# Kernel tuning notes

Measured on AMD Instinct MI355X. Metric: run time of the kernel, lower is better.

## Reference

```python
import jax, jax.numpy as jnp
import numpy as np

DIM = 1024
HEADS = 16
DIM_HEAD = 64
DIM_INNER = HEADS * DIM_HEAD  # 1024


def setup_inputs() -> dict:
    key = jax.random.key(0)
    k1, k2, k3 = jax.random.split(key, 3)
    x = jax.random.normal(k1, (2, 2048, DIM), dtype=jnp.float32)
    gamma = jnp.zeros((DIM,), dtype=jnp.float32)  # init as in module
    # store weights as [in, out] so y = x @ W (equivalent to torch Linear with W.T)
    w_qkv = jax.random.normal(k2, (DIM, DIM_INNER * 3), dtype=jnp.float32) * (DIM ** -0.5)
    w_out = jax.random.normal(k3, (DIM_INNER, DIM), dtype=jnp.float32) * (DIM_INNER ** -0.5)
    return {"x": x, "gamma": gamma, "w_qkv": w_qkv, "w_out": w_out}


def rms_norm(x, gamma):
    # F.normalize(x, dim=-1) * sqrt(dim) * (gamma + 1)
    eps = 1e-12
    norm = jnp.maximum(jnp.linalg.norm(x, axis=-1, keepdims=True), eps)
    return x / norm * (x.shape[-1] ** 0.5) * (gamma + 1.0)


def reference(x, gamma, w_qkv, w_out):
    b, n, _ = x.shape
    scale = DIM_HEAD ** -0.5
    xn = rms_norm(x, gamma)
    qkv = xn @ w_qkv  # [b, n, 3*h*d]
    qkv = qkv.reshape(b, n, 3, HEADS, DIM_HEAD)
    qkv = jnp.transpose(qkv, (2, 0, 3, 1, 4))  # [3, b, h, n, d]
    q, k, v = qkv[0], qkv[1], qkv[2]
    q = q * scale
    sim = jnp.einsum('bhid,bhjd->bhij', q, k)
    attn = jax.nn.softmax(sim, axis=-1)
    out = jnp.einsum('bhij,bhjd->bhid', attn, v)  # [b, h, n, d]
    out = jnp.transpose(out, (0, 2, 1, 3)).reshape(b, n, DIM_INNER)
    return out @ w_out
```

## Files before the change

kernel.cpp:

```cpp
#include <hip/hip_runtime.h>
#include <hip/hip_bf16.h>
#include <string.h>

typedef unsigned short ushort_t;
typedef __attribute__((ext_vector_type(8))) short short8;
typedef __attribute__((ext_vector_type(4))) short short4v;
typedef __attribute__((ext_vector_type(4))) float floatx4;
typedef __attribute__((ext_vector_type(4))) int int4v;
typedef __attribute__((ext_vector_type(4))) unsigned short us4;

#define MFMA(a, b, c) __builtin_amdgcn_mfma_f32_16x16x32_bf16(a, b, c, 0, 0, 0)
#define MFMA16(a, b, c) __builtin_amdgcn_mfma_f32_16x16x16bf16_1k(a, b, c, 0, 0, 0)

__device__ __forceinline__ float b2f(ushort_t u) {
    union { float f; unsigned i; } c; c.i = ((unsigned)u) << 16; return c.f;
}
__device__ __forceinline__ ushort_t f2b(float f) {
    union { float f; unsigned i; } c; c.f = f;
    unsigned r = c.i + 0x7FFFu + ((c.i >> 16) & 1u);
    return (ushort_t)(r >> 16);
}
__device__ __forceinline__ unsigned pk_bf16(float a, float b) {
    float2 f; f.x = a; f.y = b;
    __hip_bfloat162 h = __float22bfloat162_rn(f);
    unsigned u;
    memcpy(&u, &h, 4);
    return u;
}
__device__ __forceinline__ void gl_lds16(const ushort_t* g, ushort_t* l) {
    __builtin_amdgcn_global_load_lds(
        (const __attribute__((address_space(1))) void*)g,
        (__attribute__((address_space(3))) void*)l, 16, 0, 0);
}

__global__ __launch_bounds__(256) void rmsnorm_k(const float* __restrict__ x,
                                                 const float* __restrict__ gamma,
                                                 ushort_t* __restrict__ xn) {
    int row = blockIdx.x;
    const float* xr = x + (size_t)row * 1024;
    ushort_t* orow = xn + (size_t)row * 1024;
    int t = threadIdx.x;

    floatx4 u = *(const floatx4*)&xr[t * 4];
    float ss = u[0] * u[0] + u[1] * u[1] + u[2] * u[2] + u[3] * u[3];
    #pragma unroll
    for (int off = 32; off; off >>= 1) ss += __shfl_xor(ss, off);
    __shared__ float red[4];
    if ((t & 63) == 0) red[t >> 6] = ss;
    __syncthreads();
    float tot = red[0] + red[1] + red[2] + red[3];
    float inv = rsqrtf(fmaxf(tot, 1e-24f)) * 32.0f;

    floatx4 g = *(const floatx4*)&gamma[t * 4];
    us4 o;
    o.x = f2b(u[0] * inv * (1.0f + g[0]));
    o.y = f2b(u[1] * inv * (1.0f + g[1]));
    o.z = f2b(u[2] * inv * (1.0f + g[2]));
    o.w = f2b(u[3] * inv * (1.0f + g[3]));
    *(us4*)&orow[t * 4] = o;
}

__global__ __launch_bounds__(256) void transpose_cvt2_k(const float* __restrict__ wq,
                                                        ushort_t* __restrict__ oq,
                                                        const float* __restrict__ wo,
                                                        ushort_t* __restrict__ oo) {
    __shared__ ushort_t Ts[64 * 72];
    int bid = blockIdx.x;
    const float* in; ushort_t* out; int K, N, n0, k0;
    if (bid < 768) { in = wq; out = oq; K = 1024; N = 3072;
                     n0 = (bid % 48) * 64; k0 = (bid / 48) * 64; }
    else           { int b2 = bid - 768; in = wo; out = oo; K = 1024; N = 1024;
                     n0 = (b2 & 15) * 64; k0 = (b2 >> 4) * 64; }
    int t = threadIdx.x;
    #pragma unroll
    for (int i = 0; i < 4; i++) {
        int idx = t + i * 256;
        int r = idx >> 4, g = idx & 15;
        floatx4 v = *(const floatx4*)&in[(size_t)(k0 + r) * N + n0 + g * 4];
        us4 o; o.x = f2b(v[0]); o.y = f2b(v[1]); o.z = f2b(v[2]); o.w = f2b(v[3]);
        *(us4*)&Ts[r * 72 + g * 4] = o;
    }
    __syncthreads();
    #pragma unroll
    for (int i = 0; i < 2; i++) {
        int idx = t + i * 256;
        int r = idx >> 3, g = idx & 7;
        ushort_t tmp[8];
        #pragma unroll
        for (int j = 0; j < 8; j++) tmp[j] = Ts[(g * 8 + j) * 72 + r];
        *(int4v*)&out[(size_t)(n0 + r) * K + k0 + g * 8] = *(const int4v*)tmp;
    }
}

template <bool F32OUT>
__global__ __launch_bounds__(256) void gemm_tn(const ushort_t* __restrict__ A,
                                               const ushort_t* __restrict__ Bt,
                                               void* __restrict__ Cv,
                                               int M, int N, int K) {
    __shared__ ushort_t As[128 * 64];
    __shared__ ushort_t Bs[128 * 64];
    int t = threadIdx.x;
    int m0 = blockIdx.y * 128, n0 = blockIdx.x * 128;
    int lane = t & 63, wave = t >> 6, quad = lane >> 4, l16 = lane & 15;
    int wm = (wave & 1) * 64, wn = (wave >> 1) * 64;
    floatx4 acc[4][4] = {};

    int srow = lane >> 3;
    int schunk = (lane & 7) ^ srow;
    const ushort_t* Ag = A + (size_t)(m0 + wave * 8 + srow) * K + schunk * 8;
    const ushort_t* Bg = Bt + (size_t)(n0 + wave * 8 + srow) * K + schunk * 8;
    int lbase = (wave * 8) * 64;

    int xq = l16 & 7;

    for (int k1 = 0; k1 < K; k1 += 64) {
        #pragma unroll
        for (int i = 0; i < 4; i++) {
            gl_lds16(Ag + (size_t)(i * 32) * K + k1, &As[lbase + i * 32 * 64]);
            gl_lds16(Bg + (size_t)(i * 32) * K + k1, &Bs[lbase + i * 32 * 64]);
        }
        __syncthreads();
        #pragma unroll
        for (int ks = 0; ks < 2; ks++) {
            int ca = ((ks * 4 + quad) ^ xq) * 8;
            short8 af[4], bf[4];
            #pragma unroll
            for (int i = 0; i < 4; i++) {
                af[i] = *(const short8*)&As[(wm + i * 16 + l16) * 64 + ca];
                bf[i] = *(const short8*)&Bs[(wn + i * 16 + l16) * 64 + ca];
            }
            #pragma unroll
            for (int mt = 0; mt < 4; mt++)
                #pragma unroll
                for (int nt = 0; nt < 4; nt++)
                    acc[mt][nt] = MFMA(af[mt], bf[nt], acc[mt][nt]);
        }
        __syncthreads();
    }
    #pragma unroll
    for (int mt = 0; mt < 4; mt++)
        #pragma unroll
        for (int r = 0; r < 4; r++) {
            int row = m0 + wm + mt * 16 + quad * 4 + r;
            #pragma unroll
            for (int nt = 0; nt < 4; nt++) {
                int col = n0 + wn + nt * 16 + l16;
                if constexpr (F32OUT)
                    ((float*)Cv)[(size_t)row * N + col] = acc[mt][nt][r];
                else
                    ((ushort_t*)Cv)[(size_t)row * N + col] = f2b(acc[mt][nt][r]);
            }
        }
}

#define LDA 72
__global__ __launch_bounds__(256, 2) void attn_k(const ushort_t* __restrict__ qk,
                                                 const ushort_t* __restrict__ vT,
                                                 ushort_t* __restrict__ o) {
    __shared__ ushort_t Ks[64 * LDA];
    __shared__ ushort_t Vt[64 * LDA];
    int t = threadIdx.x;
    int lane = t & 63, wave = t >> 6, quad = lane >> 4, l16 = lane & 15;
    int bid = blockIdx.x;
    int bh = bid & 31, qb = bid >> 5;
    int b = bh >> 4, h = bh & 15;
    int q0 = qb * 128 + wave * 32;
    const size_t RS = 2048;
    const ushort_t* Qb = qk + (size_t)b * 2048 * RS + h * 64;
    const ushort_t* Kb = Qb + 1024;
    const ushort_t* Vb = vT + (size_t)(h * 64) * 4096 + b * 2048;
    const float SC = 0.18033688011112042f;

    int srow = t >> 2, sseg = t & 3;
    const ushort_t* Kg = Kb + (size_t)srow * RS + sseg * 8;
    const ushort_t* Vg = Vb + (size_t)srow * 4096 + sseg * 8;

    short8 qf[2][2];
    #pragma unroll
    for (int qt = 0; qt < 2; qt++)
        #pragma unroll
        for (int ks = 0; ks < 2; ks++) {
            union { short8 s; ushort_t u[8]; } a;
            a.s = *(const short8*)&Qb[(size_t)(q0 + qt * 16 + l16) * RS + ks * 32 + quad * 8];
            #pragma unroll
            for (int j = 0; j < 8; j++) a.u[j] = f2b(b2f(a.u[j]) * SC);
            qf[qt][ks] = a.s;
        }

    short4v ones4;
    #pragma unroll
    for (int j = 0; j < 4; j++) ones4[j] = (short)0x3F80;

    floatx4 oacc[2][4] = {};
    floatx4 sum_acc[2] = {};

    int4v kr0 = *(const int4v*)Kg;
    int4v kr1 = *(const int4v*)(Kg + 32);
    int4v vr0 = *(const int4v*)Vg;
    int4v vr1 = *(const int4v*)(Vg + 32);

    for (int kt = 0; kt < 2048; kt += 64) {
        __syncthreads();
        *(int4v*)&Ks[srow * LDA + sseg * 8] = kr0;
        *(int4v*)&Ks[srow * LDA + 32 + sseg * 8] = kr1;
        *(int4v*)&Vt[srow * LDA + sseg * 8] = vr0;
        *(int4v*)&Vt[srow * LDA + 32 + sseg * 8] = vr1;
        __syncthreads();

        if (kt + 64 < 2048) {
            const ushort_t* Kg2 = Kg + (size_t)(kt + 64) * RS;
            const ushort_t* Vg2 = Vg + (kt + 64);
            kr0 = *(const int4v*)Kg2;
            kr1 = *(const int4v*)(Kg2 + 32);
            vr0 = *(const int4v*)Vg2;
            vr1 = *(const int4v*)(Vg2 + 32);
        }

        floatx4 s[2][4];
        #pragma unroll
        for (int mt = 0; mt < 4; mt++) {
            short8 kf0 = *(const short8*)&Ks[(mt * 16 + l16) * LDA + quad * 8];
            short8 kf1 = *(const short8*)&Ks[(mt * 16 + l16) * LDA + 32 + quad * 8];
            #pragma unroll
            for (int qt = 0; qt < 2; qt++) {
                floatx4 z = {};
                z = MFMA(kf0, qf[qt][0], z);
                s[qt][mt] = MFMA(kf1, qf[qt][1], z);
            }
        }

        short4v pa[2][4];
        #pragma unroll
        for (int qt = 0; qt < 2; qt++)
            #pragma unroll
            for (int mt = 0; mt < 4; mt++) {
                union { short4v v; unsigned u[2]; } pk;
                pk.u[0] = pk_bf16(exp2f(s[qt][mt][0]), exp2f(s[qt][mt][1]));
                pk.u[1] = pk_bf16(exp2f(s[qt][mt][2]), exp2f(s[qt][mt][3]));
                pa[qt][mt] = pk.v;
            }

        #pragma unroll
        for (int mt = 0; mt < 4; mt++) {
            short4v vb[4];
            #pragma unroll
            for (int dt = 0; dt < 4; dt++)
                vb[dt] = *(const short4v*)&Vt[(dt * 16 + l16) * LDA + mt * 16 + quad * 4];
            #pragma unroll
            for (int qt = 0; qt < 2; qt++) {
                sum_acc[qt] = MFMA16(pa[qt][mt], ones4, sum_acc[qt]);
                #pragma unroll
                for (int dt = 0; dt < 4; dt++)
                    oacc[qt][dt] = MFMA16(pa[qt][mt], vb[dt], oacc[qt][dt]);
            }
        }
    }

    ushort_t* ob = o + (size_t)b * 2048 * 1024 + h * 64;
    #pragma unroll
    for (int qt = 0; qt < 2; qt++)
        #pragma unroll
        for (int r = 0; r < 4; r++) {
            float inv = 1.0f / sum_acc[qt][r];
            int row = q0 + qt * 16 + quad * 4 + r;
            #pragma unroll
            for (int dt = 0; dt < 4; dt++)
                ob[(size_t)row * 1024 + dt * 16 + l16] = f2b(oacc[qt][dt][r] * inv);
        }
}

extern "C" void kernel_launch(void* const* d_in, const int* in_sizes, int n_in,
                              void* d_out, int out_size, void* d_ws, size_t ws_size,
                              hipStream_t stream) {
    const float* x     = (const float*)d_in[0];
    const float* gamma = (const float*)d_in[1];
    const float* w_qkv = (const float*)d_in[2];
    const float* w_out = (const float*)d_in[3];
    float* out = (float*)d_out;

    ushort_t* ws   = (ushort_t*)d_ws;
    ushort_t* xn   = ws;
    ushort_t* qkb  = xn + (size_t)4096 * 1024;
    ushort_t* vTb  = qkb + (size_t)4096 * 2048;
    ushort_t* wtq  = vTb + (size_t)1024 * 4096;
    ushort_t* wto  = wtq + (size_t)3072 * 1024;
    ushort_t* attn = xn;

    rmsnorm_k<<<4096, 256, 0, stream>>>(x, gamma, xn);
    transpose_cvt2_k<<<1024, 256, 0, stream>>>(w_qkv, wtq, w_out, wto);
    gemm_tn<false><<<dim3(16, 32), 256, 0, stream>>>(xn, wtq, qkb, 4096, 2048, 1024);
    gemm_tn<false><<<dim3(32, 8), 256, 0, stream>>>(wtq + (size_t)2048 * 1024, xn, vTb,
                                                    1024, 4096, 1024);
    attn_k<<<512, 256, 0, stream>>>(qkb, vTb, attn);
    gemm_tn<true><<<dim3(8, 32), 256, 0, stream>>>(attn, wto, out, 4096, 1024, 1024);
}
```

Measured before the change: 218.8 us.

## Fuse QKV GEMM, transpose V separately, split attention keys across two wave groups

```diff
diff --git a/kernel.cpp b/kernel.cpp
--- a/kernel.cpp
+++ b/kernel.cpp
@@ -92,6 +92,32 @@
     }
 }
 
+__global__ __launch_bounds__(256) void transpose_v_k(const ushort_t* __restrict__ qkv,
+                                                     ushort_t* __restrict__ vT) {
+    __shared__ ushort_t Ts[64 * 72];
+    int t = threadIdx.x;
+    int t0 = blockIdx.x * 64;
+    int c0 = blockIdx.y * 64;
+    const ushort_t* in = qkv + 2048 + c0;
+    #pragma unroll
+    for (int i = 0; i < 2; i++) {
+        int idx = t + i * 256;
+        int r = idx >> 3, g = idx & 7;
+        *(int4v*)&Ts[r * 72 + g * 8] =
+            *(const int4v*)&in[(size_t)(t0 + r) * 3072 + g * 8];
+    }
+    __syncthreads();
+    #pragma unroll
+    for (int i = 0; i < 2; i++) {
+        int idx = t + i * 256;
+        int r = idx >> 3, g = idx & 7;
+        ushort_t tmp[8];
+        #pragma unroll
+        for (int j = 0; j < 8; j++) tmp[j] = Ts[(g * 8 + j) * 72 + r];
+        *(int4v*)&vT[(size_t)(c0 + r) * 4096 + t0 + g * 8] = *(const int4v*)tmp;
+    }
+}
+
 template <bool F32OUT>
 __global__ __launch_bounds__(256) void gemm_tn(const ushort_t* __restrict__ A,
                                                const ushort_t* __restrict__ Bt,
@@ -110,7 +136,6 @@
     const ushort_t* Ag = A + (size_t)(m0 + wave * 8 + srow) * K + schunk * 8;
     const ushort_t* Bg = Bt + (size_t)(n0 + wave * 8 + srow) * K + schunk * 8;
     int lbase = (wave * 8) * 64;
-
     int xq = l16 & 7;
 
     for (int k1 = 0; k1 < K; k1 += 64) {
@@ -154,26 +179,31 @@
 }
 
 #define LDA 72
-__global__ __launch_bounds__(256, 2) void attn_k(const ushort_t* __restrict__ qk,
+__global__ __launch_bounds__(512, 4) void attn_k(const ushort_t* __restrict__ qkv,
                                                  const ushort_t* __restrict__ vT,
                                                  ushort_t* __restrict__ o) {
-    __shared__ ushort_t Ks[64 * LDA];
-    __shared__ ushort_t Vt[64 * LDA];
+    __shared__ ushort_t S[4][64 * LDA];
     int t = threadIdx.x;
     int lane = t & 63, wave = t >> 6, quad = lane >> 4, l16 = lane & 15;
+    int half = wave >> 2, w4 = wave & 3;
     int bid = blockIdx.x;
     int bh = bid & 31, qb = bid >> 5;
     int b = bh >> 4, h = bh & 15;
-    int q0 = qb * 128 + wave * 32;
-    const size_t RS = 2048;
-    const ushort_t* Qb = qk + (size_t)b * 2048 * RS + h * 64;
+    int q0 = qb * 128 + w4 * 32;
+    const size_t RS = 3072;
+    const ushort_t* Qb = qkv + (size_t)b * 2048 * RS + h * 64;
     const ushort_t* Kb = Qb + 1024;
     const ushort_t* Vb = vT + (size_t)(h * 64) * 4096 + b * 2048;
     const float SC = 0.18033688011112042f;
 
-    int srow = t >> 2, sseg = t & 3;
-    const ushort_t* Kg = Kb + (size_t)srow * RS + sseg * 8;
-    const ushort_t* Vg = Vb + (size_t)srow * 4096 + sseg * 8;
+    ushort_t* Ks = S[half * 2];
+    ushort_t* Vt = S[half * 2 + 1];
+
+    int ht = t & 255;
+    int srow = ht >> 2, sseg = ht & 3;
+    int kbase = half * 1024;
+    const ushort_t* Kg = Kb + (size_t)(kbase + srow) * RS + sseg * 8;
+    const ushort_t* Vg = Vb + (size_t)srow * 4096 + kbase + sseg * 8;
 
     short8 qf[2][2];
     #pragma unroll
@@ -199,7 +229,7 @@
     int4v vr0 = *(const int4v*)Vg;
     int4v vr1 = *(const int4v*)(Vg + 32);
 
-    for (int kt = 0; kt < 2048; kt += 64) {
+    for (int kt = 0; kt < 1024; kt += 64) {
         __syncthreads();
         *(int4v*)&Ks[srow * LDA + sseg * 8] = kr0;
         *(int4v*)&Ks[srow * LDA + 32 + sseg * 8] = kr1;
@@ -207,7 +237,7 @@
         *(int4v*)&Vt[srow * LDA + 32 + sseg * 8] = vr1;
         __syncthreads();
 
-        if (kt + 64 < 2048) {
+        if (kt + 64 < 1024) {
             const ushort_t* Kg2 = Kg + (size_t)(kt + 64) * RS;
             const ushort_t* Vg2 = Vg + (kt + 64);
             kr0 = *(const int4v*)Kg2;
@@ -256,17 +286,43 @@
         }
     }
 
-    ushort_t* ob = o + (size_t)b * 2048 * 1024 + h * 64;
-    #pragma unroll
-    for (int qt = 0; qt < 2; qt++)
-        #pragma unroll
-        for (int r = 0; r < 4; r++) {
-            float inv = 1.0f / sum_acc[qt][r];
-            int row = q0 + qt * 16 + quad * 4 + r;
+    float* xb = (float*)&S[0][0];
+    int ci = (w4 * 64 + lane) * 20;
+    #pragma unroll
+    for (int qt = 0; qt < 2; qt++) {
+        __syncthreads();
+        if (half == 1) {
             #pragma unroll
             for (int dt = 0; dt < 4; dt++)
-                ob[(size_t)row * 1024 + dt * 16 + l16] = f2b(oacc[qt][dt][r] * inv);
-        }
+                #pragma unroll
+                for (int r = 0; r < 4; r++) xb[ci + dt * 4 + r] = oacc[qt][dt][r];
+            #pragma unroll
+            for (int r = 0; r < 4; r++) xb[ci + 16 + r] = sum_acc[qt][r];
+        }
+        __syncthreads();
+        if (half == 0) {
+            #pragma unroll
+            for (int dt = 0; dt < 4; dt++)
+                #pragma unroll
+                for (int r = 0; r < 4; r++) oacc[qt][dt][r] += xb[ci + dt * 4 + r];
+            #pragma unroll
+            for (int r = 0; r < 4; r++) sum_acc[qt][r] += xb[ci + 16 + r];
+        }
+    }
+
+    if (half == 0) {
+        ushort_t* ob = o + (size_t)b * 2048 * 1024 + h * 64;
+        #pragma unroll
+        for (int qt = 0; qt < 2; qt++)
+            #pragma unroll
+            for (int r = 0; r < 4; r++) {
+                float inv = 1.0f / sum_acc[qt][r];
+                int row = q0 + qt * 16 + quad * 4 + r;
+                #pragma unroll
+                for (int dt = 0; dt < 4; dt++)
+                    ob[(size_t)row * 1024 + dt * 16 + l16] = f2b(oacc[qt][dt][r] * inv);
+            }
+    }
 }
 
 extern "C" void kernel_launch(void* const* d_in, const int* in_sizes, int n_in,
@@ -280,17 +336,16 @@
 
     ushort_t* ws   = (ushort_t*)d_ws;
     ushort_t* xn   = ws;
-    ushort_t* qkb  = xn + (size_t)4096 * 1024;
-    ushort_t* vTb  = qkb + (size_t)4096 * 2048;
+    ushort_t* qkv  = xn + (size_t)4096 * 1024;
+    ushort_t* vTb  = qkv + (size_t)4096 * 3072;
     ushort_t* wtq  = vTb + (size_t)1024 * 4096;
     ushort_t* wto  = wtq + (size_t)3072 * 1024;
     ushort_t* attn = xn;
 
     rmsnorm_k<<<4096, 256, 0, stream>>>(x, gamma, xn);
     transpose_cvt2_k<<<1024, 256, 0, stream>>>(w_qkv, wtq, w_out, wto);
-    gemm_tn<false><<<dim3(16, 32), 256, 0, stream>>>(xn, wtq, qkb, 4096, 2048, 1024);
-    gemm_tn<false><<<dim3(32, 8), 256, 0, stream>>>(wtq + (size_t)2048 * 1024, xn, vTb,
-                                                    1024, 4096, 1024);
-    attn_k<<<512, 256, 0, stream>>>(qkb, vTb, attn);
+    gemm_tn<false><<<dim3(24, 32), 256, 0, stream>>>(xn, wtq, qkv, 4096, 3072, 1024);
+    transpose_v_k<<<dim3(64, 16), 256, 0, stream>>>(qkv, vTb);
+    attn_k<<<512, 512, 0, stream>>>(qkv, vTb, attn);
     gemm_tn<true><<<dim3(8, 32), 256, 0, stream>>>(attn, wto, out, 4096, 1024, 1024);
 }
```

New measurement: 227.1 us. 1.04x slower.

## Merge QK and V projections into one GEMM, add V transpose kernel, use fast exp2

Applied to the files above, without the earlier changes.

```diff
diff --git a/kernel.cpp b/kernel.cpp
--- a/kernel.cpp
+++ b/kernel.cpp
@@ -11,6 +11,7 @@
 
 #define MFMA(a, b, c) __builtin_amdgcn_mfma_f32_16x16x32_bf16(a, b, c, 0, 0, 0)
 #define MFMA16(a, b, c) __builtin_amdgcn_mfma_f32_16x16x16bf16_1k(a, b, c, 0, 0, 0)
+#define EXP2(x) __builtin_amdgcn_exp2f(x)
 
 __device__ __forceinline__ float b2f(ushort_t u) {
     union { float f; unsigned i; } c; c.i = ((unsigned)u) << 16; return c.f;
@@ -92,6 +93,32 @@
     }
 }
 
+__global__ __launch_bounds__(256) void transpose_v_k(const ushort_t* __restrict__ qkv,
+                                                     ushort_t* __restrict__ vT) {
+    __shared__ ushort_t Ts[64 * 72];
+    int t = threadIdx.x;
+    int t0 = blockIdx.x * 64;
+    int c0 = blockIdx.y * 64;
+    const ushort_t* in = qkv + 2048 + c0;
+    #pragma unroll
+    for (int i = 0; i < 2; i++) {
+        int idx = t + i * 256;
+        int r = idx >> 3, g = idx & 7;
+        *(int4v*)&Ts[r * 72 + g * 8] =
+            *(const int4v*)&in[(size_t)(t0 + r) * 3072 + g * 8];
+    }
+    __syncthreads();
+    #pragma unroll
+    for (int i = 0; i < 2; i++) {
+        int idx = t + i * 256;
+        int r = idx >> 3, g = idx & 7;
+        ushort_t tmp[8];
+        #pragma unroll
+        for (int j = 0; j < 8; j++) tmp[j] = Ts[(g * 8 + j) * 72 + r];
+        *(int4v*)&vT[(size_t)(c0 + r) * 4096 + t0 + g * 8] = *(const int4v*)tmp;
+    }
+}
+
 template <bool F32OUT>
 __global__ __launch_bounds__(256) void gemm_tn(const ushort_t* __restrict__ A,
                                                const ushort_t* __restrict__ Bt,
@@ -110,7 +137,6 @@
     const ushort_t* Ag = A + (size_t)(m0 + wave * 8 + srow) * K + schunk * 8;
     const ushort_t* Bg = Bt + (size_t)(n0 + wave * 8 + srow) * K + schunk * 8;
     int lbase = (wave * 8) * 64;
-
     int xq = l16 & 7;
 
     for (int k1 = 0; k1 < K; k1 += 64) {
@@ -154,7 +180,7 @@
 }
 
 #define LDA 72
-__global__ __launch_bounds__(256, 2) void attn_k(const ushort_t* __restrict__ qk,
+__global__ __launch_bounds__(256, 2) void attn_k(const ushort_t* __restrict__ qkv,
                                                  const ushort_t* __restrict__ vT,
                                                  ushort_t* __restrict__ o) {
     __shared__ ushort_t Ks[64 * LDA];
@@ -165,8 +191,8 @@
     int bh = bid & 31, qb = bid >> 5;
     int b = bh >> 4, h = bh & 15;
     int q0 = qb * 128 + wave * 32;
-    const size_t RS = 2048;
-    const ushort_t* Qb = qk + (size_t)b * 2048 * RS + h * 64;
+    const size_t RS = 3072;
+    const ushort_t* Qb = qkv + (size_t)b * 2048 * RS + h * 64;
     const ushort_t* Kb = Qb + 1024;
     const ushort_t* Vb = vT + (size_t)(h * 64) * 4096 + b * 2048;
     const float SC = 0.18033688011112042f;
@@ -235,8 +261,8 @@
             #pragma unroll
             for (int mt = 0; mt < 4; mt++) {
                 union { short4v v; unsigned u[2]; } pk;
-                pk.u[0] = pk_bf16(exp2f(s[qt][mt][0]), exp2f(s[qt][mt][1]));
-                pk.u[1] = pk_bf16(exp2f(s[qt][mt][2]), exp2f(s[qt][mt][3]));
+                pk.u[0] = pk_bf16(EXP2(s[qt][mt][0]), EXP2(s[qt][mt][1]));
+                pk.u[1] = pk_bf16(EXP2(s[qt][mt][2]), EXP2(s[qt][mt][3]));
                 pa[qt][mt] = pk.v;
             }
 
@@ -280,17 +306,16 @@
 
     ushort_t* ws   = (ushort_t*)d_ws;
     ushort_t* xn   = ws;
-    ushort_t* qkb  = xn + (size_t)4096 * 1024;
-    ushort_t* vTb  = qkb + (size_t)4096 * 2048;
+    ushort_t* qkv  = xn + (size_t)4096 * 1024;
+    ushort_t* vTb  = qkv + (size_t)4096 * 3072;
     ushort_t* wtq  = vTb + (size_t)1024 * 4096;
     ushort_t* wto  = wtq + (size_t)3072 * 1024;
     ushort_t* attn = xn;
 
     rmsnorm_k<<<4096, 256, 0, stream>>>(x, gamma, xn);
     transpose_cvt2_k<<<1024, 256, 0, stream>>>(w_qkv, wtq, w_out, wto);
-    gemm_tn<false><<<dim3(16, 32), 256, 0, stream>>>(xn, wtq, qkb, 4096, 2048, 1024);
-    gemm_tn<false><<<dim3(32, 8), 256, 0, stream>>>(wtq + (size_t)2048 * 1024, xn, vTb,
-                                                    1024, 4096, 1024);
-    attn_k<<<512, 256, 0, stream>>>(qkb, vTb, attn);
+    gemm_tn<false><<<dim3(24, 32), 256, 0, stream>>>(xn, wtq, qkv, 4096, 3072, 1024);
+    transpose_v_k<<<dim3(64, 16), 256, 0, stream>>>(qkv, vTb);
+    attn_k<<<512, 256, 0, stream>>>(qkv, vTb, attn);
     gemm_tn<true><<<dim3(8, 32), 256, 0, stream>>>(attn, wto, out, 4096, 1024, 1024);
 }
```

Result: faster. 194.0 us (-11.3%).
